# Kernel tuning notes

Hardware: AMD Instinct MI355X
Metric: run time of the kernel (lower is better)

The kernel has to match this reference:

```python
import jax, jax.numpy as jnp
import numpy as np

EPS = 1e-4
HEAD_DIM = 64
MP_T = 0.3


def _mp_conv1x1(x, w):
    # Magnitude-preserving 1x1 conv: weight is normalized per output filter
    # (torch: normalize(w) / sqrt(fan_in), with normalize using
    #  alpha = sqrt(n.numel()/w.numel()) = 1/sqrt(fan_in)).
    O, I, kh, kw = w.shape
    fan_in = I * kh * kw
    n = jnp.sqrt(jnp.sum(w * w, axis=(1, 2, 3), keepdims=True))  # [O,1,1,1]
    alpha = 1.0 / np.sqrt(fan_in)
    wn = w / (EPS + alpha * n) / np.sqrt(fan_in)
    # 1x1 'same' conv == channel matmul
    return jnp.einsum('oi,bihw->bohw', wn[:, :, 0, 0], x)


def _pixel_norm(x):
    # torch pixel_norm with default dim=1: normalize over axis 1 (the heads axis
    # for q/k/v of shape [b, heads, seq, head_dim]) -- faithful to source.
    return x * jax.lax.rsqrt(jnp.mean(x * x, axis=1, keepdims=True) + EPS)


def setup_inputs() -> dict:
    key = jax.random.key(0)
    k1, k2, k3 = jax.random.split(key, 3)
    b, c, h, w = 16, 512, 32, 32
    return {
        'x': jax.random.normal(k1, (b, c, h, w), dtype=jnp.float32),
        'w_attn': jax.random.normal(k2, (3 * c, c, 1, 1), dtype=jnp.float32),
        'w_proj': jax.random.normal(k3, (c, c, 1, 1), dtype=jnp.float32),
    }


def reference(x, w_attn, w_proj):
    b, c, h, w = x.shape
    hd = HEAD_DIM
    nh = c // hd
    seq = h * w

    x_proj = _mp_conv1x1(x, w_attn)                      # [b, 3c, h, w]
    x_proj = x_proj.reshape(b, 3 * c, seq).transpose(0, 2, 1)  # [b, seq, 3c]
    q, k, v = jnp.split(x_proj, 3, axis=-1)              # each [b, seq, c]

    def to_heads(t):
        return t.reshape(b, seq, nh, hd).transpose(0, 2, 1, 3)  # [b, nh, seq, hd]

    q, k, v = _pixel_norm(to_heads(q)), _pixel_norm(to_heads(k)), _pixel_norm(to_heads(v))

    # scaled dot product attention (no mask)
    scale = 1.0 / np.sqrt(hd)
    scores = jnp.einsum('bnqd,bnkd->bnqk', q, k) * scale
    attn = jax.nn.softmax(scores, axis=-1)
    res = jnp.einsum('bnqk,bnkd->bnqd', attn, v)         # [b, nh, seq, hd]

    # transpose(-1,-2) then reshape(b, -1, h, w): [b, nh, hd, seq] -> [b, c, h, w]
    res = res.transpose(0, 1, 3, 2).reshape(b, c, h, w)
    res = _mp_conv1x1(res, w_proj)

    # mp_add(input, res, t=0.3)
    t = MP_T
    scale_add = np.sqrt(t * t + (1 - t) ** 2)
    return ((1 - t) * x + t * res) / scale_add
```

## Files before the change

kernel.cpp:

```cpp
#include <hip/hip_runtime.h>
#include <hip/hip_bf16.h>


typedef __attribute__((ext_vector_type(8))) short short8;
typedef __attribute__((ext_vector_type(8))) unsigned short ushort8;
typedef __attribute__((ext_vector_type(4))) float f32x4;
typedef __attribute__((ext_vector_type(16))) float f32x16;
typedef __attribute__((ext_vector_type(4))) unsigned int uint4_t;

__device__ inline unsigned short f2bf(float v) {
  __hip_bfloat16 h = __float2bfloat16(v);
  return *reinterpret_cast<unsigned short*>(&h);
}
__device__ inline float bf2f(unsigned short u) {
  return __uint_as_float((unsigned)u << 16);
}
__device__ inline unsigned cvt_pk(float lo, float hi) {
  unsigned r;
  asm("v_cvt_pk_bf16_f32 %0, %1, %2" : "=v"(r) : "v"(lo), "v"(hi));
  return r;
}
__device__ inline float fexp2(float x) {
#if __has_builtin(__builtin_amdgcn_exp2f)
  return __builtin_amdgcn_exp2f(x);
#else
  float r;
  asm("v_exp_f32 %0, %1\n\ts_nop 0" : "=v"(r) : "v"(x));
  return r;
#endif
}
__device__ inline float frsq(float x) {
#if __has_builtin(__builtin_amdgcn_rsqf)
  return __builtin_amdgcn_rsqf(x);
#else
  return rsqrtf(x);
#endif
}
__device__ inline void gload16(const void* g, void* l) {
  __builtin_amdgcn_global_load_lds(
      (const __attribute__((address_space(1))) unsigned int*)g,
      (__attribute__((address_space(3))) unsigned int*)l, 16, 0, 0);
}

__global__ __launch_bounds__(256) void wnorm_kernel(
    const float* __restrict__ wa, const float* __restrict__ wp,
    __hip_bfloat16* __restrict__ wna, __hip_bfloat16* __restrict__ wnp) {
  int o = blockIdx.x;
  const float* src;
  __hip_bfloat16* dst;
  if (o < 1536) {
    int g = o >> 9, rem = o & 511, n = rem >> 6, d = rem & 63;
    int row = g * 512 + (d >> 4) * 128 + n * 16 + (d & 15);
    src = wa + (size_t)o * 512;
    dst = wna + (size_t)row * 512;
  } else {
    src = wp + (size_t)(o - 1536) * 512;
    dst = wnp + (size_t)(o - 1536) * 512;
  }
  int tid = threadIdx.x;
  float a = src[tid], b = src[tid + 256];
  float ss = a * a + b * b;
#pragma unroll
  for (int off = 32; off > 0; off >>= 1) ss += __shfl_down(ss, off, 64);
  __shared__ float wsum[4];
  if ((tid & 63) == 0) wsum[tid >> 6] = ss;
  __syncthreads();
  float tot = wsum[0] + wsum[1] + wsum[2] + wsum[3];
  float r = 1.0f / (sqrtf(tot) + 2.2627416997969522e-3f);
  dst[tid] = __float2bfloat16(a * r);
  dst[tid + 256] = __float2bfloat16(b * r);
}

__global__ __launch_bounds__(256) void xt_kernel(
    const float* __restrict__ x, __hip_bfloat16* __restrict__ xt) {
  __shared__ __align__(16) unsigned short trans[64][68];
  int s0 = blockIdx.x * 64, c0 = blockIdx.y * 64, b = blockIdx.z;
  int t = threadIdx.x;
  int sl = t & 63, cg = t >> 6;
  const float* src = x + (size_t)b * 524288 + (size_t)(c0 + cg * 16) * 1024 + s0 + sl;
#pragma unroll
  for (int i = 0; i < 16; i += 2) {
    float v0 = src[(size_t)i * 1024];
    float v1 = src[(size_t)(i + 1) * 1024];
    *(unsigned*)&trans[sl][cg * 16 + i] = (unsigned)f2bf(v0) | ((unsigned)f2bf(v1) << 16);
  }
  __syncthreads();
  int sw = t >> 2, cw = (t & 3) * 16;
  __hip_bfloat16* dst = xt + (size_t)b * 524288 + (size_t)(s0 + sw) * 512 + c0 + cw;
  uint2 r0 = *(uint2*)&trans[sw][cw + 0];
  uint2 r1 = *(uint2*)&trans[sw][cw + 4];
  uint2 r2 = *(uint2*)&trans[sw][cw + 8];
  uint2 r3 = *(uint2*)&trans[sw][cw + 12];
  uint4 o0 = {r0.x, r0.y, r1.x, r1.y};
  uint4 o1 = {r2.x, r2.y, r3.x, r3.y};
  *(uint4*)dst = o0;
  *(uint4*)((char*)dst + 16) = o1;
}

__global__ __launch_bounds__(256) void gemm_qkv(
    const __hip_bfloat16* __restrict__ A, const __hip_bfloat16* __restrict__ B,
    __hip_bfloat16* __restrict__ q_sd, __hip_bfloat16* __restrict__ k_sd,
    __hip_bfloat16* __restrict__ v_ds) {
  __shared__ __align__(16) char smem[65536];
  char* AlB = smem;
  char* BlB = smem + 32768;
  int t = threadIdx.x;
  int w = t >> 6, l = t & 63;
  int l15 = l & 15, lg = l >> 4;
  int wm = w >> 1, wn = w & 1;
  int bid = blockIdx.x;
  int xcd = bid & 7;
  int idx = bid >> 3;
  int b = xcd * 2 + (idx >= 96 ? 1 : 0);
  int r = idx >= 96 ? idx - 96 : idx;
  int mt = r >> 3;
  int n0 = (r & 7) * 128;
  int m0 = mt * 128;
  int g = mt >> 2, dq = mt & 3;

  const char* Ab = (const char*)A + (size_t)m0 * 1024;
  const char* Bb = (const char*)B + (size_t)b * 1048576 + (size_t)n0 * 1024;
  int rl = t >> 3;
  int soff = ((t & 7) * 16) ^ ((rl & 7) << 4);
  const char* asrc = Ab + (size_t)rl * 1024 + soff;
  const char* bsrc = Bb + (size_t)rl * 1024 + soff;

#define STAGE(bi, k0b)                                                       \
  do {                                                                       \
    _Pragma("unroll") for (int i = 0; i < 4; ++i) {                          \
      gload16(asrc + (size_t)i * 32768 + (k0b), AlB + (bi)*16384 + i * 4096 + w * 1024); \
      gload16(bsrc + (size_t)i * 32768 + (k0b), BlB + (bi)*16384 + i * 4096 + w * 1024); \
    }                                                                        \
  } while (0)

  f32x4 acc[4][4];
#pragma unroll
  for (int mi = 0; mi < 4; ++mi)
#pragma unroll
    for (int ni = 0; ni < 4; ++ni) acc[mi][ni] = (f32x4){0.f, 0.f, 0.f, 0.f};

  STAGE(0, 0);
  __syncthreads();

  for (int ks = 0; ks < 8; ++ks) {
    int buf = ks & 1;
    if (ks < 7) STAGE(buf ^ 1, (ks + 1) * 128);
    short8 af[4][2], bf[4][2];
#pragma unroll
    for (int mi = 0; mi < 4; ++mi) {
      int row = wm * 64 + mi * 16 + l15;
      int sw = (row & 7) << 4;
#pragma unroll
      for (int h = 0; h < 2; ++h)
        af[mi][h] = *(const short8*)(AlB + buf * 16384 + row * 128 + ((h * 64 + lg * 16) ^ sw));
    }
#pragma unroll
    for (int ni = 0; ni < 4; ++ni) {
      int row = wn * 64 + ni * 16 + l15;
      int sw = (row & 7) << 4;
#pragma unroll
      for (int h = 0; h < 2; ++h)
        bf[ni][h] = *(const short8*)(BlB + buf * 16384 + row * 128 + ((h * 64 + lg * 16) ^ sw));
    }
    __builtin_amdgcn_s_setprio(1);
#pragma unroll
    for (int mi = 0; mi < 4; ++mi)
#pragma unroll
      for (int ni = 0; ni < 4; ++ni) {
        acc[mi][ni] = __builtin_amdgcn_mfma_f32_16x16x32_bf16(af[mi][0], bf[ni][0], acc[mi][ni], 0, 0, 0);
        acc[mi][ni] = __builtin_amdgcn_mfma_f32_16x16x32_bf16(af[mi][1], bf[ni][1], acc[mi][ni], 0, 0, 0);
      }
    __builtin_amdgcn_s_setprio(0);
    if (ks < 7) __syncthreads();
  }
#undef STAGE

  __syncthreads();

  if (g < 2) {
    unsigned short(*LT)[136] = (unsigned short(*)[136])smem;
#pragma unroll
    for (int mi = 0; mi < 4; ++mi)
#pragma unroll
      for (int ni = 0; ni < 4; ++ni) {
        int sl = wn * 64 + ni * 16 + l15;
        int lr0 = wm * 64 + mi * 16 + lg * 4;
        *(unsigned*)&LT[sl][lr0] = cvt_pk(acc[mi][ni][0], acc[mi][ni][1]);
        *(unsigned*)&LT[sl][lr0 + 2] = cvt_pk(acc[mi][ni][2], acc[mi][ni][3]);
      }
    __syncthreads();
    int s = t >> 1, dd8 = (t & 1) * 8;
    ushort8 v[8];
#pragma unroll
    for (int n = 0; n < 8; ++n) v[n] = *(ushort8*)&LT[s][n * 16 + dd8];
    float f[8];
#pragma unroll
    for (int j = 0; j < 8; ++j) {
      float ss = 0.f;
#pragma unroll
      for (int n = 0; n < 8; ++n) { float xv = bf2f(v[n][j]); ss += xv * xv; }
      f[j] = frsq(ss * 0.125f + 1e-4f);
    }
    if (g == 0) {
#pragma unroll
      for (int j = 0; j < 8; ++j) f[j] *= 0.18033688011112042f;
    }
    unsigned short* dstb = (unsigned short*)(g ? k_sd : q_sd) +
        ((size_t)(b * 8) * 1024 + n0 + s) * 64 + dq * 16 + dd8;
#pragma unroll
    for (int n = 0; n < 8; ++n) {
      uint4 o;
      o.x = cvt_pk(bf2f(v[n][0]) * f[0], bf2f(v[n][1]) * f[1]);
      o.y = cvt_pk(bf2f(v[n][2]) * f[2], bf2f(v[n][3]) * f[3]);
      o.z = cvt_pk(bf2f(v[n][4]) * f[4], bf2f(v[n][5]) * f[5]);
      o.w = cvt_pk(bf2f(v[n][6]) * f[6], bf2f(v[n][7]) * f[7]);
      *(uint4*)(dstb + (size_t)n * 65536) = o;
    }
  } else {
    unsigned short(*L)[136] = (unsigned short(*)[136])smem;
#pragma unroll
    for (int mi = 0; mi < 4; ++mi)
#pragma unroll
      for (int ni = 0; ni < 4; ++ni) {
        int sl = wn * 64 + ni * 16 + l15;
        int lr0 = wm * 64 + mi * 16 + lg * 4;
#pragma unroll
        for (int rr = 0; rr < 4; ++rr) L[lr0 + rr][sl] = f2bf(acc[mi][ni][rr]);
      }
    __syncthreads();
    int dd = t >> 4, s0 = (t & 15) * 8;
    ushort8 v[8];
#pragma unroll
    for (int n = 0; n < 8; ++n) v[n] = *(ushort8*)&L[n * 16 + dd][s0];
    float f[8];
#pragma unroll
    for (int j = 0; j < 8; ++j) {
      float ss = 0.f;
#pragma unroll
      for (int n = 0; n < 8; ++n) { float xv = bf2f(v[n][j]); ss += xv * xv; }
      f[j] = frsq(ss * 0.125f + 1e-4f);
    }
    unsigned short* dstb = (unsigned short*)v_ds +
        ((size_t)(b * 8) * 64 + dq * 16 + dd) * 1024 + n0 + s0;
#pragma unroll
    for (int n = 0; n < 8; ++n) {
      uint4 o;
      o.x = cvt_pk(bf2f(v[n][0]) * f[0], bf2f(v[n][1]) * f[1]);
      o.y = cvt_pk(bf2f(v[n][2]) * f[2], bf2f(v[n][3]) * f[3]);
      o.z = cvt_pk(bf2f(v[n][4]) * f[4], bf2f(v[n][5]) * f[5]);
      o.w = cvt_pk(bf2f(v[n][6]) * f[6], bf2f(v[n][7]) * f[7]);
      *(uint4*)(dstb + (size_t)n * 65536) = o;
    }
  }
}

template <int MODE>
__global__ __launch_bounds__(256) void gemm_bf16(
    const __hip_bfloat16* __restrict__ A, const __hip_bfloat16* __restrict__ B,
    void* __restrict__ Outv, const float* __restrict__ resid, int M) {
  __shared__ __align__(16) char Al[2][16384];
  __shared__ __align__(16) char Bl[2][16384];
  int t = threadIdx.x;
  int w = t >> 6, l = t & 63;
  int l15 = l & 15, lg = l >> 4;
  int wm = w >> 1, wn = w & 1;
  int bid = blockIdx.x;
  int mt = M >> 7;
  int half = mt * 8;
  int xcd = bid & 7;
  int idx = bid >> 3;
  int b = xcd * 2 + (idx >= half ? 1 : 0);
  int r = idx >= half ? idx - half : idx;
  int m0 = (r >> 3) * 128, n0 = (r & 7) * 128;

  const char* Ab = (const char*)A + (size_t)m0 * 1024;
  const char* Bb = (const char*)B + (size_t)b * 1048576 + (size_t)n0 * 1024;
  int rl = t >> 3;
  int soff = ((t & 7) * 16) ^ ((rl & 7) << 4);
  const char* asrc = Ab + (size_t)rl * 1024 + soff;
  const char* bsrc = Bb + (size_t)rl * 1024 + soff;

#define STAGE(bi, k0b)                                                    \
  do {                                                                    \
    _Pragma("unroll") for (int i = 0; i < 4; ++i) {                       \
      gload16(asrc + (size_t)i * 32768 + (k0b), Al[bi] + i * 4096 + w * 1024); \
      gload16(bsrc + (size_t)i * 32768 + (k0b), Bl[bi] + i * 4096 + w * 1024); \
    }                                                                     \
  } while (0)

  f32x4 acc[4][4];
#pragma unroll
  for (int mi = 0; mi < 4; ++mi)
#pragma unroll
    for (int ni = 0; ni < 4; ++ni) acc[mi][ni] = (f32x4){0.f, 0.f, 0.f, 0.f};

  STAGE(0, 0);
  __syncthreads();

  for (int ks = 0; ks < 8; ++ks) {
    int buf = ks & 1;
    if (ks < 7) STAGE(buf ^ 1, (ks + 1) * 128);
    short8 af[4][2], bf[4][2];
#pragma unroll
    for (int mi = 0; mi < 4; ++mi) {
      int row = wm * 64 + mi * 16 + l15;
      int sw = (row & 7) << 4;
#pragma unroll
      for (int h = 0; h < 2; ++h)
        af[mi][h] = *(const short8*)(Al[buf] + row * 128 + ((h * 64 + lg * 16) ^ sw));
    }
#pragma unroll
    for (int ni = 0; ni < 4; ++ni) {
      int row = wn * 64 + ni * 16 + l15;
      int sw = (row & 7) << 4;
#pragma unroll
      for (int h = 0; h < 2; ++h)
        bf[ni][h] = *(const short8*)(Bl[buf] + row * 128 + ((h * 64 + lg * 16) ^ sw));
    }
    __builtin_amdgcn_s_setprio(1);
#pragma unroll
    for (int mi = 0; mi < 4; ++mi)
#pragma unroll
      for (int ni = 0; ni < 4; ++ni) {
        acc[mi][ni] = __builtin_amdgcn_mfma_f32_16x16x32_bf16(af[mi][0], bf[ni][0], acc[mi][ni], 0, 0, 0);
        acc[mi][ni] = __builtin_amdgcn_mfma_f32_16x16x32_bf16(af[mi][1], bf[ni][1], acc[mi][ni], 0, 0, 0);
      }
    __builtin_amdgcn_s_setprio(0);
    if (ks < 7) __syncthreads();
  }
#undef STAGE

  float* outb = (float*)Outv + (size_t)b * M * 1024;
  const float* rb = resid + (size_t)b * M * 1024;
#pragma unroll
  for (int mi = 0; mi < 4; ++mi) {
    int row = m0 + wm * 64 + mi * 16 + lg * 4;
#pragma unroll
    for (int rr = 0; rr < 4; ++rr) {
      float* orow = outb + (size_t)(row + rr) * 1024 + n0 + wn * 64 + l15;
      const float* rrow = rb + (size_t)(row + rr) * 1024 + n0 + wn * 64 + l15;
#pragma unroll
      for (int ni = 0; ni < 4; ++ni)
        orow[ni * 16] = 0.9191450300180578f * rrow[ni * 16] +
                        0.39391929857916763f * acc[mi][ni][rr];
    }
  }
}

__global__ __launch_bounds__(512, 4) void attn_mfma(
    const __hip_bfloat16* __restrict__ q_sd, const __hip_bfloat16* __restrict__ k_sd,
    const __hip_bfloat16* __restrict__ v_ds, __hip_bfloat16* __restrict__ y_t) {
  __shared__ __align__(16) char K_lds[2][8192];
  __shared__ __align__(16) char V_lds[2][8192];
  int t = threadIdx.x;
  int w = t >> 6, l = t & 63;
  int l31 = l & 31, h5 = l >> 5;
  int swV = (l31 & 7) << 4;
  int pl = (l31 & 0x13) | ((l31 & 4) << 1) | ((l31 & 8) >> 1);
  int swK = (pl & 7) << 4;
  int bn = blockIdx.x, qb = blockIdx.y;
  const char* qg = (const char*)(q_sd + (size_t)bn * 65536);
  const char* kg = (const char*)(k_sd + (size_t)bn * 65536);
  const char* vg = (const char*)(v_ds + (size_t)bn * 65536);

  int q = qb * 256 + w * 32 + l31;
  short8 bq[4];
#pragma unroll
  for (int j = 0; j < 4; ++j)
    bq[j] = *(const short8*)(qg + (size_t)q * 128 + j * 32 + h5 * 16);

  f32x16 o_acc[2];
#pragma unroll
  for (int r = 0; r < 16; ++r) { o_acc[0][r] = 0.f; o_acc[1][r] = 0.f; }
  float l_run = 0.f;

  int rowS = t >> 3;
  int offS = (t & 7) * 16;
  int swrS = (rowS & 7) << 4;
  {
    uint4 a = *(const uint4*)(kg + (size_t)t * 16);
    uint4 b2 = *(const uint4*)(vg + (size_t)rowS * 2048 + offS);
    *(uint4*)(K_lds[0] + ((t * 16) ^ swrS)) = a;
    *(uint4*)(V_lds[0] + ((t * 16) ^ swrS)) = b2;
  }
  __syncthreads();

  for (int kb = 0; kb < 16; ++kb) {
    int buf = kb & 1;
    uint4 pk, pv;
    if (kb < 15) {
      pk = *(const uint4*)(kg + (size_t)(kb + 1) * 8192 + (size_t)t * 16);
      pv = *(const uint4*)(vg + (size_t)rowS * 2048 + (size_t)(kb + 1) * 128 + offS);
    }
    short8 a_k[2][4];
#pragma unroll
    for (int kt = 0; kt < 2; ++kt)
#pragma unroll
      for (int j = 0; j < 4; ++j)
        a_k[kt][j] = *(const short8*)(K_lds[buf] +
            (((kt * 32 + pl) * 128 + j * 32 + h5 * 16) ^ swK));
    f32x16 s0, s1;
#pragma unroll
    for (int r = 0; r < 16; ++r) { s0[r] = 0.f; s1[r] = 0.f; }
    __builtin_amdgcn_s_setprio(1);
#pragma unroll
    for (int j = 0; j < 4; ++j) {
      s0 = __builtin_amdgcn_mfma_f32_32x32x16_bf16(a_k[0][j], bq[j], s0, 0, 0, 0);
      s1 = __builtin_amdgcn_mfma_f32_32x32x16_bf16(a_k[1][j], bq[j], s1, 0, 0, 0);
    }
    __builtin_amdgcn_s_setprio(0);
    unsigned W0[8], W1[8];
    float ts = 0.f;
#pragma unroll
    for (int m = 0; m < 8; ++m) {
      float p0 = fexp2(s0[2 * m]), p1 = fexp2(s0[2 * m + 1]);
      float p2 = fexp2(s1[2 * m]), p3 = fexp2(s1[2 * m + 1]);
      ts += (p0 + p1) + (p2 + p3);
      W0[m] = cvt_pk(p0, p1);
      W1[m] = cvt_pk(p2, p3);
    }
    l_run += ts;
    short8 pb[4];
#pragma unroll
    for (int j = 0; j < 4; ++j) {
      uint4_t pw;
      if (j == 0)      pw = (uint4_t){W0[0], W0[1], W0[2], W0[3]};
      else if (j == 1) pw = (uint4_t){W0[4], W0[5], W0[6], W0[7]};
      else if (j == 2) pw = (uint4_t){W1[0], W1[1], W1[2], W1[3]};
      else             pw = (uint4_t){W1[4], W1[5], W1[6], W1[7]};
      pb[j] = __builtin_bit_cast(short8, pw);
    }
    short8 a_v[2][4];
#pragma unroll
    for (int dt = 0; dt < 2; ++dt)
#pragma unroll
      for (int j = 0; j < 4; ++j)
        a_v[dt][j] = *(const short8*)(V_lds[buf] +
            (((dt * 32 + l31) * 128 + j * 32 + h5 * 16) ^ swV));
    __builtin_amdgcn_s_setprio(1);
#pragma unroll
    for (int j = 0; j < 4; ++j) {
      o_acc[0] = __builtin_amdgcn_mfma_f32_32x32x16_bf16(a_v[0][j], pb[j], o_acc[0], 0, 0, 0);
      o_acc[1] = __builtin_amdgcn_mfma_f32_32x32x16_bf16(a_v[1][j], pb[j], o_acc[1], 0, 0, 0);
    }
    __builtin_amdgcn_s_setprio(0);
    if (kb < 15) {
      int nb = buf ^ 1;
      *(uint4*)(K_lds[nb] + ((t * 16) ^ swrS)) = pk;
      *(uint4*)(V_lds[nb] + ((t * 16) ^ swrS)) = pv;
    }
    __syncthreads();
  }
  int b_ = bn >> 3, n_ = bn & 7;
  float lsum = l_run + __shfl_xor(l_run, 32, 64);
  float invl = 1.0f / lsum;
  __hip_bfloat16* yrow = y_t + (size_t)b_ * 524288 + (size_t)q * 512 + n_ * 64 + h5 * 4;
#pragma unroll
  for (int dt = 0; dt < 2; ++dt) {
#pragma unroll
    for (int g4 = 0; g4 < 4; ++g4) {
      uint2 pr;
      pr.x = cvt_pk(o_acc[dt][4 * g4 + 0] * invl, o_acc[dt][4 * g4 + 1] * invl);
      pr.y = cvt_pk(o_acc[dt][4 * g4 + 2] * invl, o_acc[dt][4 * g4 + 3] * invl);
      *(uint2*)(yrow + dt * 32 + g4 * 8) = pr;
    }
  }
}

extern "C" void kernel_launch(void* const* d_in, const int* in_sizes, int n_in,
                              void* d_out, int out_size, void* d_ws, size_t ws_size,
                              hipStream_t stream) {
  const float* x      = (const float*)d_in[0];
  const float* w_attn = (const float*)d_in[1];
  const float* w_proj = (const float*)d_in[2];
  float* out = (float*)d_out;

  __hip_bfloat16* wn_attn = (__hip_bfloat16*)d_ws;
  __hip_bfloat16* wn_proj = wn_attn + 786432;
  __hip_bfloat16* x_t     = wn_proj + 262144;
  __hip_bfloat16* y_t     = x_t;
  __hip_bfloat16* q_sd    = x_t + 8388608;
  __hip_bfloat16* k_sd    = q_sd + 8388608;
  __hip_bfloat16* v_ds    = k_sd + 8388608;

  wnorm_kernel<<<dim3(2048), dim3(256), 0, stream>>>(w_attn, w_proj, wn_attn, wn_proj);
  xt_kernel<<<dim3(16, 8, 16), dim3(256), 0, stream>>>(x, x_t);
  gemm_qkv<<<dim3(1536), dim3(256), 0, stream>>>(wn_attn, x_t, q_sd, k_sd, v_ds);
  attn_mfma<<<dim3(128, 4), dim3(512), 0, stream>>>(q_sd, k_sd, v_ds, y_t);
  gemm_bf16<1><<<dim3(512), dim3(256), 0, stream>>>(wn_proj, y_t, out, x, 512);
}
```

Measured before the change: 121.0 us.

## Process two 32-query tiles per wave in attention to reuse K/V LDS reads

The attention kernel now runs 4 waves per block instead of 8. Each wave handles 64 queries as two 32-row halves, reusing the same K and V fragments read from LDS for both halves. This halves LDS read traffic per query and the number of waves sharing each block barrier. In exchange each thread holds roughly twice the accumulators and Q fragments and loads twice as much data per staging step, which raises register pressure and may lower occupancy.

```diff
diff --git a/kernel.cpp b/kernel.cpp
--- a/kernel.cpp
+++ b/kernel.cpp
@@ -347,7 +347,7 @@
   }
 }
 
-__global__ __launch_bounds__(512, 4) void attn_mfma(
+__global__ __launch_bounds__(256, 2) void attn_mfma(
     const __hip_bfloat16* __restrict__ q_sd, const __hip_bfloat16* __restrict__ k_sd,
     const __hip_bfloat16* __restrict__ v_ds, __hip_bfloat16* __restrict__ y_t) {
   __shared__ __align__(16) char K_lds[2][8192];
@@ -363,34 +363,50 @@
   const char* kg = (const char*)(k_sd + (size_t)bn * 65536);
   const char* vg = (const char*)(v_ds + (size_t)bn * 65536);
 
-  int q = qb * 256 + w * 32 + l31;
-  short8 bq[4];
-#pragma unroll
-  for (int j = 0; j < 4; ++j)
-    bq[j] = *(const short8*)(qg + (size_t)q * 128 + j * 32 + h5 * 16);
-
-  f32x16 o_acc[2];
-#pragma unroll
-  for (int r = 0; r < 16; ++r) { o_acc[0][r] = 0.f; o_acc[1][r] = 0.f; }
-  float l_run = 0.f;
-
-  int rowS = t >> 3;
-  int offS = (t & 7) * 16;
+  int q0 = qb * 256 + w * 64 + l31;
+  short8 bq[2][4];
+#pragma unroll
+  for (int qh = 0; qh < 2; ++qh)
+#pragma unroll
+    for (int j = 0; j < 4; ++j)
+      bq[qh][j] = *(const short8*)(qg + (size_t)(q0 + qh * 32) * 128 + j * 32 + h5 * 16);
+
+  f32x16 o_acc[2][2];
+#pragma unroll
+  for (int qh = 0; qh < 2; ++qh)
+#pragma unroll
+    for (int dt = 0; dt < 2; ++dt)
+#pragma unroll
+      for (int r = 0; r < 16; ++r) o_acc[qh][dt][r] = 0.f;
+  float l_run[2] = {0.f, 0.f};
+
+  int rowS = t >> 2;
+  int coff = (t & 3) * 32;
   int swrS = (rowS & 7) << 4;
   {
-    uint4 a = *(const uint4*)(kg + (size_t)t * 16);
-    uint4 b2 = *(const uint4*)(vg + (size_t)rowS * 2048 + offS);
-    *(uint4*)(K_lds[0] + ((t * 16) ^ swrS)) = a;
-    *(uint4*)(V_lds[0] + ((t * 16) ^ swrS)) = b2;
+    const char* ksrc = kg + (size_t)t * 32;
+    const char* vsrc = vg + (size_t)rowS * 2048 + coff;
+    uint4 a0 = *(const uint4*)(ksrc);
+    uint4 a1 = *(const uint4*)(ksrc + 16);
+    uint4 b0 = *(const uint4*)(vsrc);
+    uint4 b1 = *(const uint4*)(vsrc + 16);
+    *(uint4*)(K_lds[0] + ((t * 32) ^ swrS)) = a0;
+    *(uint4*)(K_lds[0] + ((t * 32 + 16) ^ swrS)) = a1;
+    *(uint4*)(V_lds[0] + ((t * 32) ^ swrS)) = b0;
+    *(uint4*)(V_lds[0] + ((t * 32 + 16) ^ swrS)) = b1;
   }
   __syncthreads();
 
   for (int kb = 0; kb < 16; ++kb) {
     int buf = kb & 1;
-    uint4 pk, pv;
+    uint4 pk0, pk1, pv0, pv1;
     if (kb < 15) {
-      pk = *(const uint4*)(kg + (size_t)(kb + 1) * 8192 + (size_t)t * 16);
-      pv = *(const uint4*)(vg + (size_t)rowS * 2048 + (size_t)(kb + 1) * 128 + offS);
+      const char* ksrc = kg + (size_t)(kb + 1) * 8192 + (size_t)t * 32;
+      const char* vsrc = vg + (size_t)rowS * 2048 + (size_t)(kb + 1) * 128 + coff;
+      pk0 = *(const uint4*)(ksrc);
+      pk1 = *(const uint4*)(ksrc + 16);
+      pv0 = *(const uint4*)(vsrc);
+      pv1 = *(const uint4*)(vsrc + 16);
     }
     short8 a_k[2][4];
 #pragma unroll
@@ -399,36 +415,39 @@
       for (int j = 0; j < 4; ++j)
         a_k[kt][j] = *(const short8*)(K_lds[buf] +
             (((kt * 32 + pl) * 128 + j * 32 + h5 * 16) ^ swK));
-    f32x16 s0, s1;
-#pragma unroll
-    for (int r = 0; r < 16; ++r) { s0[r] = 0.f; s1[r] = 0.f; }
-    __builtin_amdgcn_s_setprio(1);
-#pragma unroll
-    for (int j = 0; j < 4; ++j) {
-      s0 = __builtin_amdgcn_mfma_f32_32x32x16_bf16(a_k[0][j], bq[j], s0, 0, 0, 0);
-      s1 = __builtin_amdgcn_mfma_f32_32x32x16_bf16(a_k[1][j], bq[j], s1, 0, 0, 0);
-    }
-    __builtin_amdgcn_s_setprio(0);
-    unsigned W0[8], W1[8];
-    float ts = 0.f;
-#pragma unroll
-    for (int m = 0; m < 8; ++m) {
-      float p0 = fexp2(s0[2 * m]), p1 = fexp2(s0[2 * m + 1]);
-      float p2 = fexp2(s1[2 * m]), p3 = fexp2(s1[2 * m + 1]);
-      ts += (p0 + p1) + (p2 + p3);
-      W0[m] = cvt_pk(p0, p1);
-      W1[m] = cvt_pk(p2, p3);
-    }
-    l_run += ts;
-    short8 pb[4];
-#pragma unroll
-    for (int j = 0; j < 4; ++j) {
-      uint4_t pw;
-      if (j == 0)      pw = (uint4_t){W0[0], W0[1], W0[2], W0[3]};
-      else if (j == 1) pw = (uint4_t){W0[4], W0[5], W0[6], W0[7]};
-      else if (j == 2) pw = (uint4_t){W1[0], W1[1], W1[2], W1[3]};
-      else             pw = (uint4_t){W1[4], W1[5], W1[6], W1[7]};
-      pb[j] = __builtin_bit_cast(short8, pw);
+    short8 pb[2][4];
+#pragma unroll
+    for (int qh = 0; qh < 2; ++qh) {
+      f32x16 s0, s1;
+#pragma unroll
+      for (int r = 0; r < 16; ++r) { s0[r] = 0.f; s1[r] = 0.f; }
+      __builtin_amdgcn_s_setprio(1);
+#pragma unroll
+      for (int j = 0; j < 4; ++j) {
+        s0 = __builtin_amdgcn_mfma_f32_32x32x16_bf16(a_k[0][j], bq[qh][j], s0, 0, 0, 0);
+        s1 = __builtin_amdgcn_mfma_f32_32x32x16_bf16(a_k[1][j], bq[qh][j], s1, 0, 0, 0);
+      }
+      __builtin_amdgcn_s_setprio(0);
+      unsigned W0[8], W1[8];
+      float ts = 0.f;
+#pragma unroll
+      for (int m = 0; m < 8; ++m) {
+        float p0 = fexp2(s0[2 * m]), p1 = fexp2(s0[2 * m + 1]);
+        float p2 = fexp2(s1[2 * m]), p3 = fexp2(s1[2 * m + 1]);
+        ts += (p0 + p1) + (p2 + p3);
+        W0[m] = cvt_pk(p0, p1);
+        W1[m] = cvt_pk(p2, p3);
+      }
+      l_run[qh] += ts;
+#pragma unroll
+      for (int j = 0; j < 4; ++j) {
+        uint4_t pw;
+        if (j == 0)      pw = (uint4_t){W0[0], W0[1], W0[2], W0[3]};
+        else if (j == 1) pw = (uint4_t){W0[4], W0[5], W0[6], W0[7]};
+        else if (j == 2) pw = (uint4_t){W1[0], W1[1], W1[2], W1[3]};
+        else             pw = (uint4_t){W1[4], W1[5], W1[6], W1[7]};
+        pb[qh][j] = __builtin_bit_cast(short8, pw);
+      }
     }
     short8 a_v[2][4];
 #pragma unroll
@@ -439,30 +458,38 @@
             (((dt * 32 + l31) * 128 + j * 32 + h5 * 16) ^ swV));
     __builtin_amdgcn_s_setprio(1);
 #pragma unroll
-    for (int j = 0; j < 4; ++j) {
-      o_acc[0] = __builtin_amdgcn_mfma_f32_32x32x16_bf16(a_v[0][j], pb[j], o_acc[0], 0, 0, 0);
-      o_acc[1] = __builtin_amdgcn_mfma_f32_32x32x16_bf16(a_v[1][j], pb[j], o_acc[1], 0, 0, 0);
-    }
+    for (int qh = 0; qh < 2; ++qh)
+#pragma unroll
+      for (int j = 0; j < 4; ++j) {
+        o_acc[qh][0] = __builtin_amdgcn_mfma_f32_32x32x16_bf16(a_v[0][j], pb[qh][j], o_acc[qh][0], 0, 0, 0);
+        o_acc[qh][1] = __builtin_amdgcn_mfma_f32_32x32x16_bf16(a_v[1][j], pb[qh][j], o_acc[qh][1], 0, 0, 0);
+      }
     __builtin_amdgcn_s_setprio(0);
     if (kb < 15) {
       int nb = buf ^ 1;
-      *(uint4*)(K_lds[nb] + ((t * 16) ^ swrS)) = pk;
-      *(uint4*)(V_lds[nb] + ((t * 16) ^ swrS)) = pv;
+      *(uint4*)(K_lds[nb] + ((t * 32) ^ swrS)) = pk0;
+      *(uint4*)(K_lds[nb] + ((t * 32 + 16) ^ swrS)) = pk1;
+      *(uint4*)(V_lds[nb] + ((t * 32) ^ swrS)) = pv0;
+      *(uint4*)(V_lds[nb] + ((t * 32 + 16) ^ swrS)) = pv1;
     }
     __syncthreads();
   }
   int b_ = bn >> 3, n_ = bn & 7;
-  float lsum = l_run + __shfl_xor(l_run, 32, 64);
-  float invl = 1.0f / lsum;
-  __hip_bfloat16* yrow = y_t + (size_t)b_ * 524288 + (size_t)q * 512 + n_ * 64 + h5 * 4;
-#pragma unroll
-  for (int dt = 0; dt < 2; ++dt) {
-#pragma unroll
-    for (int g4 = 0; g4 < 4; ++g4) {
-      uint2 pr;
-      pr.x = cvt_pk(o_acc[dt][4 * g4 + 0] * invl, o_acc[dt][4 * g4 + 1] * invl);
-      pr.y = cvt_pk(o_acc[dt][4 * g4 + 2] * invl, o_acc[dt][4 * g4 + 3] * invl);
-      *(uint2*)(yrow + dt * 32 + g4 * 8) = pr;
+#pragma unroll
+  for (int qh = 0; qh < 2; ++qh) {
+    float lsum = l_run[qh] + __shfl_xor(l_run[qh], 32, 64);
+    float invl = 1.0f / lsum;
+    int q = q0 + qh * 32;
+    __hip_bfloat16* yrow = y_t + (size_t)b_ * 524288 + (size_t)q * 512 + n_ * 64 + h5 * 4;
+#pragma unroll
+    for (int dt = 0; dt < 2; ++dt) {
+#pragma unroll
+      for (int g4 = 0; g4 < 4; ++g4) {
+        uint2 pr;
+        pr.x = cvt_pk(o_acc[qh][dt][4 * g4 + 0] * invl, o_acc[qh][dt][4 * g4 + 1] * invl);
+        pr.y = cvt_pk(o_acc[qh][dt][4 * g4 + 2] * invl, o_acc[qh][dt][4 * g4 + 3] * invl);
+        *(uint2*)(yrow + dt * 32 + g4 * 8) = pr;
+      }
     }
   }
 }
@@ -486,6 +513,6 @@
   wnorm_kernel<<<dim3(2048), dim3(256), 0, stream>>>(w_attn, w_proj, wn_attn, wn_proj);
   xt_kernel<<<dim3(16, 8, 16), dim3(256), 0, stream>>>(x, x_t);
   gemm_qkv<<<dim3(1536), dim3(256), 0, stream>>>(wn_attn, x_t, q_sd, k_sd, v_ds);
-  attn_mfma<<<dim3(128, 4), dim3(512), 0, stream>>>(q_sd, k_sd, v_ds, y_t);
+  attn_mfma<<<dim3(128, 4), dim3(256), 0, stream>>>(q_sd, k_sd, v_ds, y_t);
   gemm_bf16<1><<<dim3(512), dim3(256), 0, stream>>>(wn_proj, y_t, out, x, 512);
 }
```

Measured after the change: 135.7 us. 12.1% more time.

## Fuse weight-norm and transpose kernels; halve attention block size to 128 queries

Applied to the files above, without the earlier changes.

Merges the weight normalization and the x transpose into one prep kernel, with the block index choosing the role, which saves one launch. The attention kernel drops from 512 to 256 threads per block, each covering 128 queries, so the grid doubles to 1024 blocks and occupancy is raised to 8 blocks per CU. Each thread now loads 32 bytes of K and V per tile instead of 16. Smaller blocks give finer scheduling granularity, but each K/V tile is reloaded from global memory by twice as many blocks.

```diff
diff --git a/kernel.cpp b/kernel.cpp
--- a/kernel.cpp
+++ b/kernel.cpp
@@ -42,40 +42,43 @@
       (__attribute__((address_space(3))) unsigned int*)l, 16, 0, 0);
 }
 
-__global__ __launch_bounds__(256) void wnorm_kernel(
+__global__ __launch_bounds__(256) void prep_kernel(
     const float* __restrict__ wa, const float* __restrict__ wp,
-    __hip_bfloat16* __restrict__ wna, __hip_bfloat16* __restrict__ wnp) {
-  int o = blockIdx.x;
-  const float* src;
-  __hip_bfloat16* dst;
-  if (o < 1536) {
-    int g = o >> 9, rem = o & 511, n = rem >> 6, d = rem & 63;
-    int row = g * 512 + (d >> 4) * 128 + n * 16 + (d & 15);
-    src = wa + (size_t)o * 512;
-    dst = wna + (size_t)row * 512;
-  } else {
-    src = wp + (size_t)(o - 1536) * 512;
-    dst = wnp + (size_t)(o - 1536) * 512;
-  }
-  int tid = threadIdx.x;
-  float a = src[tid], b = src[tid + 256];
-  float ss = a * a + b * b;
-#pragma unroll
-  for (int off = 32; off > 0; off >>= 1) ss += __shfl_down(ss, off, 64);
-  __shared__ float wsum[4];
-  if ((tid & 63) == 0) wsum[tid >> 6] = ss;
-  __syncthreads();
-  float tot = wsum[0] + wsum[1] + wsum[2] + wsum[3];
-  float r = 1.0f / (sqrtf(tot) + 2.2627416997969522e-3f);
-  dst[tid] = __float2bfloat16(a * r);
-  dst[tid + 256] = __float2bfloat16(b * r);
-}
-
-__global__ __launch_bounds__(256) void xt_kernel(
+    __hip_bfloat16* __restrict__ wna, __hip_bfloat16* __restrict__ wnp,
     const float* __restrict__ x, __hip_bfloat16* __restrict__ xt) {
   __shared__ __align__(16) unsigned short trans[64][68];
-  int s0 = blockIdx.x * 64, c0 = blockIdx.y * 64, b = blockIdx.z;
+  __shared__ float wsum[4];
+  int bid = blockIdx.x;
   int t = threadIdx.x;
+  if (bid < 2048) {
+    int o = bid;
+    const float* src;
+    __hip_bfloat16* dst;
+    if (o < 1536) {
+      int g = o >> 9, rem = o & 511, n = rem >> 6, d = rem & 63;
+      int row = g * 512 + (d >> 4) * 128 + n * 16 + (d & 15);
+      src = wa + (size_t)o * 512;
+      dst = wna + (size_t)row * 512;
+    } else {
+      src = wp + (size_t)(o - 1536) * 512;
+      dst = wnp + (size_t)(o - 1536) * 512;
+    }
+    float a = src[t], b = src[t + 256];
+    float ss = a * a + b * b;
+#pragma unroll
+    for (int off = 32; off > 0; off >>= 1) ss += __shfl_down(ss, off, 64);
+    if ((t & 63) == 0) wsum[t >> 6] = ss;
+    __syncthreads();
+    float tot = wsum[0] + wsum[1] + wsum[2] + wsum[3];
+    float r = 1.0f / (sqrtf(tot) + 2.2627416997969522e-3f);
+    dst[t] = __float2bfloat16(a * r);
+    dst[t + 256] = __float2bfloat16(b * r);
+    return;
+  }
+  int bid2 = bid - 2048;
+  int s0 = (bid2 & 15) * 64;
+  int c0 = ((bid2 >> 4) & 7) * 64;
+  int b = bid2 >> 7;
   int sl = t & 63, cg = t >> 6;
   const float* src = x + (size_t)b * 524288 + (size_t)(c0 + cg * 16) * 1024 + s0 + sl;
 #pragma unroll
@@ -347,7 +350,7 @@
   }
 }
 
-__global__ __launch_bounds__(512, 4) void attn_mfma(
+__global__ __launch_bounds__(256, 8) void attn_mfma(
     const __hip_bfloat16* __restrict__ q_sd, const __hip_bfloat16* __restrict__ k_sd,
     const __hip_bfloat16* __restrict__ v_ds, __hip_bfloat16* __restrict__ y_t) {
   __shared__ __align__(16) char K_lds[2][8192];
@@ -363,7 +366,7 @@
   const char* kg = (const char*)(k_sd + (size_t)bn * 65536);
   const char* vg = (const char*)(v_ds + (size_t)bn * 65536);
 
-  int q = qb * 256 + w * 32 + l31;
+  int q = qb * 128 + w * 32 + l31;
   short8 bq[4];
 #pragma unroll
   for (int j = 0; j < 4; ++j)
@@ -374,23 +377,33 @@
   for (int r = 0; r < 16; ++r) { o_acc[0][r] = 0.f; o_acc[1][r] = 0.f; }
   float l_run = 0.f;
 
-  int rowS = t >> 3;
-  int offS = (t & 7) * 16;
+  int rowS = t >> 2;
+  int coff = (t & 3) * 32;
   int swrS = (rowS & 7) << 4;
   {
-    uint4 a = *(const uint4*)(kg + (size_t)t * 16);
-    uint4 b2 = *(const uint4*)(vg + (size_t)rowS * 2048 + offS);
-    *(uint4*)(K_lds[0] + ((t * 16) ^ swrS)) = a;
-    *(uint4*)(V_lds[0] + ((t * 16) ^ swrS)) = b2;
+    const char* ksrc = kg + (size_t)t * 32;
+    const char* vsrc = vg + (size_t)rowS * 2048 + coff;
+    uint4 a0 = *(const uint4*)(ksrc);
+    uint4 a1 = *(const uint4*)(ksrc + 16);
+    uint4 b0 = *(const uint4*)(vsrc);
+    uint4 b1 = *(const uint4*)(vsrc + 16);
+    *(uint4*)(K_lds[0] + ((t * 32) ^ swrS)) = a0;
+    *(uint4*)(K_lds[0] + ((t * 32 + 16) ^ swrS)) = a1;
+    *(uint4*)(V_lds[0] + ((t * 32) ^ swrS)) = b0;
+    *(uint4*)(V_lds[0] + ((t * 32 + 16) ^ swrS)) = b1;
   }
   __syncthreads();
 
   for (int kb = 0; kb < 16; ++kb) {
     int buf = kb & 1;
-    uint4 pk, pv;
+    uint4 pk0, pk1, pv0, pv1;
     if (kb < 15) {
-      pk = *(const uint4*)(kg + (size_t)(kb + 1) * 8192 + (size_t)t * 16);
-      pv = *(const uint4*)(vg + (size_t)rowS * 2048 + (size_t)(kb + 1) * 128 + offS);
+      const char* ksrc = kg + (size_t)(kb + 1) * 8192 + (size_t)t * 32;
+      const char* vsrc = vg + (size_t)rowS * 2048 + (size_t)(kb + 1) * 128 + coff;
+      pk0 = *(const uint4*)(ksrc);
+      pk1 = *(const uint4*)(ksrc + 16);
+      pv0 = *(const uint4*)(vsrc);
+      pv1 = *(const uint4*)(vsrc + 16);
     }
     short8 a_k[2][4];
 #pragma unroll
@@ -446,8 +459,10 @@
     __builtin_amdgcn_s_setprio(0);
     if (kb < 15) {
       int nb = buf ^ 1;
-      *(uint4*)(K_lds[nb] + ((t * 16) ^ swrS)) = pk;
-      *(uint4*)(V_lds[nb] + ((t * 16) ^ swrS)) = pv;
+      *(uint4*)(K_lds[nb] + ((t * 32) ^ swrS)) = pk0;
+      *(uint4*)(K_lds[nb] + ((t * 32 + 16) ^ swrS)) = pk1;
+      *(uint4*)(V_lds[nb] + ((t * 32) ^ swrS)) = pv0;
+      *(uint4*)(V_lds[nb] + ((t * 32 + 16) ^ swrS)) = pv1;
     }
     __syncthreads();
   }
@@ -483,9 +498,8 @@
   __hip_bfloat16* k_sd    = q_sd + 8388608;
   __hip_bfloat16* v_ds    = k_sd + 8388608;
 
-  wnorm_kernel<<<dim3(2048), dim3(256), 0, stream>>>(w_attn, w_proj, wn_attn, wn_proj);
-  xt_kernel<<<dim3(16, 8, 16), dim3(256), 0, stream>>>(x, x_t);
+  prep_kernel<<<dim3(4096), dim3(256), 0, stream>>>(w_attn, w_proj, wn_attn, wn_proj, x, x_t);
   gemm_qkv<<<dim3(1536), dim3(256), 0, stream>>>(wn_attn, x_t, q_sd, k_sd, v_ds);
-  attn_mfma<<<dim3(128, 4), dim3(512), 0, stream>>>(q_sd, k_sd, v_ds, y_t);
+  attn_mfma<<<dim3(128, 8), dim3(256), 0, stream>>>(q_sd, k_sd, v_ds, y_t);
   gemm_bf16<1><<<dim3(512), dim3(256), 0, stream>>>(wn_proj, y_t, out, x, 512);
 }
```

Result: slower. 126.6 us (+4.7%).
